# Optimization experiments

Measured on AMD Instinct MI355X. Metric: run time of the kernel, lower is better.

## Reference

```python
import jax, jax.numpy as jnp
import numpy as np

B, S, D, H = 2, 2048, 1024, 16
HD = D // H  # head size 64

def setup_inputs() -> dict:
    key = jax.random.key(0)
    ks = jax.random.split(key, 7)
    sc = 1.0 / np.sqrt(D)
    return {
        "batch_data": jax.random.normal(ks[0], (B, S, D), dtype=jnp.float32),
        "Wq": jax.random.normal(ks[1], (D, D), dtype=jnp.float32) * sc,
        "bq": jnp.zeros((D,), dtype=jnp.float32),
        "Wk": jax.random.normal(ks[2], (D, D), dtype=jnp.float32) * sc,
        "bk": jnp.zeros((D,), dtype=jnp.float32),
        "Wv": jax.random.normal(ks[3], (D, D), dtype=jnp.float32) * sc,
        "bv": jnp.zeros((D,), dtype=jnp.float32),
    }

def _split_heads(x):
    # [B,S,D] -> [B,H,S,HD]
    b, s, _ = x.shape
    return x.reshape(b, s, H, HD).transpose(0, 2, 1, 3)

def reference(batch_data, Wq, bq, Wk, bk, Wv, bv):
    q = _split_heads(batch_data @ Wq + bq)
    k = _split_heads(batch_data @ Wk + bk)
    v = _split_heads(batch_data @ Wv + bv)
    scores = jnp.einsum('bhqd,bhkd->bhqk', q, k) / jnp.sqrt(jnp.float32(HD))
    probs = jax.nn.softmax(scores, axis=-1)
    ctx = jnp.einsum('bhqk,bhkd->bhqd', probs, v)  # [B,H,S,HD]
    ctx = ctx.transpose(0, 2, 1, 3).reshape(batch_data.shape[0], batch_data.shape[1], D)
    return jnp.mean(ctx, axis=1)  # mean pool over sequence -> [B,D]
```

## Files before the change

### kernel.cpp

```cpp
#include <hip/hip_runtime.h>
#include <hip/hip_bf16.h>
#include <stdint.h>

#define B_  2
#define S_  2048
#define D_  1024
#define H_  16
#define HD_ 64

typedef __attribute__((ext_vector_type(8)))  __bf16 bf16x8;
typedef __attribute__((ext_vector_type(4)))  __bf16 bf16x4;
typedef __attribute__((ext_vector_type(2)))  __bf16 bf16x2;
typedef __attribute__((ext_vector_type(4)))  short  s16x4;
typedef __attribute__((ext_vector_type(8)))  short  s16x8;
typedef __attribute__((ext_vector_type(2)))  float  f32x2;
typedef __attribute__((ext_vector_type(4)))  float  f32x4;
typedef __attribute__((ext_vector_type(16))) float  f32x16;
typedef __attribute__((ext_vector_type(4)))  uint32_t u32x4;

#define QSCALE 0.18033688011112042f

__device__ __forceinline__ void gload16(const void* g, void* l) {
  __builtin_amdgcn_global_load_lds(
      (__attribute__((address_space(1))) void*)(uintptr_t)g,
      (__attribute__((address_space(3))) void*)(uintptr_t)l,
      16, 0, 0);
}

__device__ __forceinline__ bf16x8 cat8(s16x4 a, s16x4 b) {
  return __builtin_bit_cast(
      bf16x8, (s16x8)__builtin_shufflevector(a, b, 0, 1, 2, 3, 4, 5, 6, 7));
}

__global__ __launch_bounds__(256) void prep(
    const float* __restrict__ x, const float* __restrict__ wq,
    const float* __restrict__ wk, const float* __restrict__ wv,
    __bf16* __restrict__ xb, __bf16* __restrict__ wt, float* __restrict__ out) {
  __shared__ float tile[32][33];
  const int t = threadIdx.x;
  const int bx = blockIdx.x;
  if (bx < 4096) {
    int i = bx * 256 + t;
    float4 v = ((const float4*)x)[i];
    bf16x4 o;
    o[0] = (__bf16)v.x; o[1] = (__bf16)v.y; o[2] = (__bf16)v.z; o[3] = (__bf16)v.w;
    ((bf16x4*)xb)[i] = o;
  } else if (bx < 7168) {
    int tb = bx - 4096;
    int z = tb >> 10;
    int rem = tb & 1023;
    int n0 = (rem & 31) * 32, k0 = (rem >> 5) * 32;
    const float* w = (z == 0) ? wq : (z == 1 ? wk : wv);
    __bf16* o = wt + (size_t)z * D_ * D_;
    int tx = t & 31, ty = t >> 5;
    for (int i = 0; i < 4; ++i)
      tile[ty + 8 * i][tx] = w[(size_t)(k0 + ty + 8 * i) * D_ + n0 + tx];
    __syncthreads();
    for (int i = 0; i < 4; ++i)
      o[(size_t)(n0 + ty + 8 * i) * D_ + k0 + tx] = (__bf16)tile[tx][ty + 8 * i];
  } else {
    float4* o4 = (float4*)out;
    float4 z4 = {0.f, 0.f, 0.f, 0.f};
    o4[t] = z4;
    o4[t + 256] = z4;
  }
}

__global__ __launch_bounds__(256, 3) void gemm_qkv(
    const __bf16* __restrict__ xb, const __bf16* __restrict__ wt,
    const float* __restrict__ bq, const float* __restrict__ bk,
    const float* __restrict__ bv, __bf16* __restrict__ qh,
    __bf16* __restrict__ kh, __bf16* __restrict__ vt) {
  constexpr int K = 1024;
  constexpr int NIT = K / 32;
  __shared__ __attribute__((aligned(16))) __bf16 lA[2][128 * 32];
  __shared__ __attribute__((aligned(16))) __bf16 lB[2][128 * 32];

  const int z = blockIdx.z;
  const __bf16* w = wt + (size_t)z * K * D_;
  const float* bias = (z == 0) ? bq : (z == 1 ? bk : bv);
  const int t = threadIdx.x;
  const int lane = t & 63;
  const int wid = t >> 6;
  const int quad = lane >> 4;
  const int col = lane & 15;
  const int m0 = blockIdx.x * 128;
  const int n0 = blockIdx.y * 128;
  const int wr = (wid >> 1) * 64;
  const int wc = (wid & 1) * 64;

  const int sr0 = t >> 2;
  const int gc = (t & 3) ^ ((t >> 2) & 3);

  auto stage = [&](int kt, int buf) {
    gload16(xb + (size_t)(m0 + sr0) * K + kt * 32 + gc * 8,
            (char*)&lA[buf][0] + t * 16);
    gload16(xb + (size_t)(m0 + 64 + sr0) * K + kt * 32 + gc * 8,
            (char*)&lA[buf][0] + 4096 + t * 16);
    gload16(w + (size_t)(n0 + sr0) * K + kt * 32 + gc * 8,
            (char*)&lB[buf][0] + t * 16);
    gload16(w + (size_t)(n0 + 64 + sr0) * K + kt * 32 + gc * 8,
            (char*)&lB[buf][0] + 4096 + t * 16);
  };

  f32x4 acc[4][4] = {};

  stage(0, 0);

  if (z < 2) {
    for (int kt = 0; kt < NIT; ++kt) {
      const int cur = kt & 1;
      __syncthreads();
      if (kt + 1 < NIT) stage(kt + 1, cur ^ 1);
      bf16x8 fw[4], fx[4];
      for (int i = 0; i < 4; ++i) {
        int n = wr + i * 16 + col;
        int sl = quad ^ (n & 3);
        fw[i] = *(const bf16x8*)((const char*)&lB[cur][0] + n * 64 + sl * 16);
      }
      for (int j = 0; j < 4; ++j) {
        int m = wc + j * 16 + col;
        int sl = quad ^ (m & 3);
        fx[j] = *(const bf16x8*)((const char*)&lA[cur][0] + m * 64 + sl * 16);
      }
      for (int i = 0; i < 4; ++i)
        for (int j = 0; j < 4; ++j)
          acc[i][j] = __builtin_amdgcn_mfma_f32_16x16x32_bf16(
              fw[i], fx[j], acc[i][j], 0, 0, 0);
    }
    const float scale = (z == 0) ? QSCALE : 1.0f;
    __bf16* dst = (z == 0) ? qh : kh;
    for (int i = 0; i < 4; ++i) {
      int gnb = n0 + wr + i * 16 + quad * 4;
      float4 bi = *(const float4*)(bias + gnb);
      int h = gnb >> 6, hd = gnb & 63;
      for (int j = 0; j < 4; ++j) {
        int gm = m0 + wc + j * 16 + col;
        int b = gm >> 11, s = gm & 2047;
        bf16x4 pk;
        pk[0] = (__bf16)((acc[i][j][0] + bi.x) * scale);
        pk[1] = (__bf16)((acc[i][j][1] + bi.y) * scale);
        pk[2] = (__bf16)((acc[i][j][2] + bi.z) * scale);
        pk[3] = (__bf16)((acc[i][j][3] + bi.w) * scale);
        *(bf16x4*)(dst + ((size_t)(b * H_ + h) * S_ + s) * HD_ + hd) = pk;
      }
    }
  } else {
    for (int kt = 0; kt < NIT; ++kt) {
      const int cur = kt & 1;
      __syncthreads();
      if (kt + 1 < NIT) stage(kt + 1, cur ^ 1);
      bf16x8 fx[4], fw[4];
      for (int i = 0; i < 4; ++i) {
        int m = wr + i * 16 + col;
        int sl = quad ^ (m & 3);
        fx[i] = *(const bf16x8*)((const char*)&lA[cur][0] + m * 64 + sl * 16);
      }
      for (int j = 0; j < 4; ++j) {
        int n = wc + j * 16 + col;
        int sl = quad ^ (n & 3);
        fw[j] = *(const bf16x8*)((const char*)&lB[cur][0] + n * 64 + sl * 16);
      }
      for (int i = 0; i < 4; ++i)
        for (int j = 0; j < 4; ++j)
          acc[i][j] = __builtin_amdgcn_mfma_f32_16x16x32_bf16(
              fx[i], fw[j], acc[i][j], 0, 0, 0);
    }
    for (int i = 0; i < 4; ++i) {
      int gmb = m0 + wr + i * 16 + quad * 4;
      int b = gmb >> 11, s = gmb & 2047;
      for (int j = 0; j < 4; ++j) {
        int gn = n0 + wc + j * 16 + col;
        int h = gn >> 6, hd = gn & 63;
        float bi = bias[gn];
        bf16x4 pk;
        pk[0] = (__bf16)(acc[i][j][0] + bi);
        pk[1] = (__bf16)(acc[i][j][1] + bi);
        pk[2] = (__bf16)(acc[i][j][2] + bi);
        pk[3] = (__bf16)(acc[i][j][3] + bi);
        *(bf16x4*)(vt + ((size_t)(b * H_ + h) * HD_ + hd) * S_ + s) = pk;
      }
    }
  }
}

__global__ __launch_bounds__(256, 2) void attn1(
    const __bf16* __restrict__ qh, const __bf16* __restrict__ kh,
    const __bf16* __restrict__ vt, __bf16* __restrict__ po,
    float* __restrict__ pl) {
  __shared__ __attribute__((aligned(16))) __bf16 lK[2][64 * 64];
  __shared__ __attribute__((aligned(16))) __bf16 lV[2][64 * 64];

  const int t = threadIdx.x;
  const int lane = t & 63;
  const int half = lane >> 5;
  const int q31 = lane & 31;
  const int bh = blockIdx.x;
  const int kc = blockIdx.z;
  const int q0w = blockIdx.y * 256 + (t >> 6) * 64;

  const __bf16* qbase = qh + (size_t)bh * S_ * HD_;
  const __bf16* kbase = kh + (size_t)bh * S_ * HD_;
  const __bf16* vbase = vt + (size_t)bh * HD_ * S_;

  bf16x8 aq[2][4];
  for (int qt = 0; qt < 2; ++qt)
    for (int ks = 0; ks < 4; ++ks)
      aq[qt][ks] = *(const bf16x8*)(qbase +
          (size_t)(q0w + qt * 32 + q31) * HD_ + ks * 16 + half * 8);

  f32x16 o[2][2] = {};
  f32x2 ls[2] = {{0.f, 0.f}, {0.f, 0.f}};

  const int srow = t >> 3;
  const int sgc = (t & 7) ^ (srow & 7);

  auto stage = [&](int kt, int buf) {
    gload16(kbase + (size_t)(kt * 64 + srow) * HD_ + sgc * 8,
            (char*)&lK[buf][0] + t * 16);
    gload16(kbase + (size_t)(kt * 64 + 32 + srow) * HD_ + sgc * 8,
            (char*)&lK[buf][0] + 4096 + t * 16);
    gload16(vbase + (size_t)srow * S_ + kt * 64 + sgc * 8,
            (char*)&lV[buf][0] + t * 16);
    gload16(vbase + (size_t)(32 + srow) * S_ + kt * 64 + sgc * 8,
            (char*)&lV[buf][0] + 4096 + t * 16);
  };

  stage(kc * 16, 0);

  for (int kt0 = 0; kt0 < 16; ++kt0) {
    const int cur = kt0 & 1;
    __syncthreads();
    if (kt0 + 1 < 16) stage(kc * 16 + kt0 + 1, cur ^ 1);

    bf16x8 fk[2][4];
    s16x4  fv[2][2][4];
#pragma unroll
    for (int st = 0; st < 2; ++st) {
      const int row = st * 32 + q31;
#pragma unroll
      for (int ks = 0; ks < 4; ++ks) {
        int pos = (2 * ks + half) ^ (row & 7);
        fk[st][ks] = *(const bf16x8*)((const char*)&lK[cur][0] + row * 128 + pos * 16);
      }
    }
#pragma unroll
    for (int st = 0; st < 2; ++st)
#pragma unroll
      for (int hdt = 0; hdt < 2; ++hdt) {
        const int rowv = hdt * 32 + q31;
#pragma unroll
        for (int g = 0; g < 4; ++g) {
          int pos = (4 * st + g) ^ (rowv & 7);
          fv[st][hdt][g] = *(const s16x4*)((const char*)&lV[cur][0] + rowv * 128 +
                                           pos * 16 + half * 8);
        }
      }

#pragma unroll
    for (int st = 0; st < 2; ++st) {
      f32x16 sc0 = {}, sc1 = {};
#pragma unroll
      for (int ks = 0; ks < 4; ++ks) {
        sc0 = __builtin_amdgcn_mfma_f32_32x32x16_bf16(fk[st][ks], aq[0][ks], sc0, 0, 0, 0);
        sc1 = __builtin_amdgcn_mfma_f32_32x32x16_bf16(fk[st][ks], aq[1][ks], sc1, 0, 0, 0);
      }

      uint32_t pk0[8], pk1[8];
#pragma unroll
      for (int p = 0; p < 8; ++p) {
        float ea = __builtin_amdgcn_exp2f(sc0[2 * p]);
        float eb = __builtin_amdgcn_exp2f(sc0[2 * p + 1]);
        f32x2 e2 = {ea, eb};
        ls[0] += e2;
        uint32_t au = __builtin_bit_cast(uint32_t, ea) + 0x8000u;
        uint32_t bu = __builtin_bit_cast(uint32_t, eb) + 0x8000u;
        pk0[p] = __builtin_amdgcn_perm(bu, au, 0x07060302u);
      }
#pragma unroll
      for (int p = 0; p < 8; ++p) {
        float ea = __builtin_amdgcn_exp2f(sc1[2 * p]);
        float eb = __builtin_amdgcn_exp2f(sc1[2 * p + 1]);
        f32x2 e2 = {ea, eb};
        ls[1] += e2;
        uint32_t au = __builtin_bit_cast(uint32_t, ea) + 0x8000u;
        uint32_t bu = __builtin_bit_cast(uint32_t, eb) + 0x8000u;
        pk1[p] = __builtin_amdgcn_perm(bu, au, 0x07060302u);
      }

      u32x4 w;
      w[0] = pk0[0]; w[1] = pk0[1]; w[2] = pk0[2]; w[3] = pk0[3];
      bf16x8 fp0a = __builtin_bit_cast(bf16x8, w);
      w[0] = pk0[4]; w[1] = pk0[5]; w[2] = pk0[6]; w[3] = pk0[7];
      bf16x8 fp0b = __builtin_bit_cast(bf16x8, w);
      w[0] = pk1[0]; w[1] = pk1[1]; w[2] = pk1[2]; w[3] = pk1[3];
      bf16x8 fp1a = __builtin_bit_cast(bf16x8, w);
      w[0] = pk1[4]; w[1] = pk1[5]; w[2] = pk1[6]; w[3] = pk1[7];
      bf16x8 fp1b = __builtin_bit_cast(bf16x8, w);

#pragma unroll
      for (int hdt = 0; hdt < 2; ++hdt) {
        bf16x8 av0 = cat8(fv[st][hdt][0], fv[st][hdt][1]);
        bf16x8 av1 = cat8(fv[st][hdt][2], fv[st][hdt][3]);
        o[0][hdt] = __builtin_amdgcn_mfma_f32_32x32x16_bf16(av0, fp0a, o[0][hdt], 0, 0, 0);
        o[1][hdt] = __builtin_amdgcn_mfma_f32_32x32x16_bf16(av0, fp1a, o[1][hdt], 0, 0, 0);
        o[0][hdt] = __builtin_amdgcn_mfma_f32_32x32x16_bf16(av1, fp0b, o[0][hdt], 0, 0, 0);
        o[1][hdt] = __builtin_amdgcn_mfma_f32_32x32x16_bf16(av1, fp1b, o[1][hdt], 0, 0, 0);
      }
    }
  }

  const size_t slab = (size_t)(kc * 32 + bh) * S_;
  for (int qt = 0; qt < 2; ++qt) {
    float lq = ls[qt].x + ls[qt].y;
    float ltot = lq + __shfl_xor(lq, 32);
    const int qrow = q0w + qt * 32 + q31;
    if (half == 0) pl[slab + qrow] = ltot;
    for (int hdt = 0; hdt < 2; ++hdt)
      for (int rq = 0; rq < 4; ++rq) {
        bf16x4 pk;
        pk[0] = (__bf16)o[qt][hdt][rq * 4 + 0];
        pk[1] = (__bf16)o[qt][hdt][rq * 4 + 1];
        pk[2] = (__bf16)o[qt][hdt][rq * 4 + 2];
        pk[3] = (__bf16)o[qt][hdt][rq * 4 + 3];
        *(bf16x4*)(po + (slab + qrow) * HD_ + hdt * 32 + rq * 8 + half * 4) = pk;
      }
  }
}

__global__ __launch_bounds__(256) void attn2(const __bf16* __restrict__ po,
                                             const float* __restrict__ pl,
                                             float* __restrict__ out) {
  __shared__ float red[256];
  const int t = threadIdx.x;
  const int hd = t & 63;
  const int rgrp = t >> 6;
  const int bh = blockIdx.y;
  const int r0 = blockIdx.x * 64 + rgrp * 16;
  const size_t s0 = (size_t)bh * S_;
  const size_t s1 = (size_t)(32 + bh) * S_;
  float acc = 0.f;
#pragma unroll 4
  for (int i = 0; i < 16; ++i) {
    int row = r0 + i;
    float l = pl[s0 + row] + pl[s1 + row];
    float v = (float)po[(s0 + row) * HD_ + hd] +
              (float)po[(s1 + row) * HD_ + hd];
    acc += v / l;
  }
  red[t] = acc;
  __syncthreads();
  if (t < 64) {
    float s = red[t] + red[t + 64] + red[t + 128] + red[t + 192];
    atomicAdd(out + (size_t)(bh >> 4) * D_ + (bh & 15) * HD_ + hd,
              s * (1.0f / S_));
  }
}

extern "C" void kernel_launch(void* const* d_in, const int* in_sizes, int n_in,
                              void* d_out, int out_size, void* d_ws, size_t ws_size,
                              hipStream_t stream) {
  const float* x  = (const float*)d_in[0];
  const float* Wq = (const float*)d_in[1];
  const float* bq = (const float*)d_in[2];
  const float* Wk = (const float*)d_in[3];
  const float* bk = (const float*)d_in[4];
  const float* Wv = (const float*)d_in[5];
  const float* bv = (const float*)d_in[6];
  float* out = (float*)d_out;

  char* ws = (char*)d_ws;
  __bf16* qh = (__bf16*)(ws);
  __bf16* kh = (__bf16*)(ws + ((size_t)8  << 20));
  __bf16* vt = (__bf16*)(ws + ((size_t)16 << 20));
  __bf16* xb = (__bf16*)(ws + ((size_t)24 << 20));
  __bf16* wt = (__bf16*)(ws + ((size_t)32 << 20));
  __bf16* po = (__bf16*)(ws + ((size_t)24 << 20));
  float*  pl = (float*) (ws + ((size_t)40 << 20));

  prep<<<dim3(7169), dim3(256), 0, stream>>>(x, Wq, Wk, Wv, xb, wt, out);
  gemm_qkv<<<dim3(32, 8, 3), dim3(256), 0, stream>>>(xb, wt, bq, bk, bv, qh, kh, vt);
  attn1<<<dim3(B_ * H_, 8, 2), dim3(256), 0, stream>>>(qh, kh, vt, po, pl);
  attn2<<<dim3(32, B_ * H_), dim3(256), 0, stream>>>(po, pl, out);
}
```

Baseline: 160.0 us.

## Stage 128-key tiles per barrier in attention and raise MFMA issue priority

Result: no change. 162.8 us (+1.8%).

```diff
diff --git a/kernel.cpp b/kernel.cpp
--- a/kernel.cpp
+++ b/kernel.cpp
@@ -188,8 +188,8 @@
     const __bf16* __restrict__ qh, const __bf16* __restrict__ kh,
     const __bf16* __restrict__ vt, __bf16* __restrict__ po,
     float* __restrict__ pl) {
-  __shared__ __attribute__((aligned(16))) __bf16 lK[2][64 * 64];
-  __shared__ __attribute__((aligned(16))) __bf16 lV[2][64 * 64];
+  __shared__ __attribute__((aligned(16))) __bf16 lK[2][128 * 64];
+  __shared__ __attribute__((aligned(16))) __bf16 lV[2][64 * 128];
 
   const int t = threadIdx.x;
   const int lane = t & 63;
@@ -212,100 +212,109 @@
   f32x16 o[2][2] = {};
   f32x2 ls[2] = {{0.f, 0.f}, {0.f, 0.f}};
 
-  const int srow = t >> 3;
-  const int sgc = (t & 7) ^ (srow & 7);
+  const int rK = t >> 3;
+  const int cK = (t & 7) ^ (rK & 7);
+  const int rV = t >> 4;
+  const int cV = (t & 15) ^ (rV & 7);
 
   auto stage = [&](int kt, int buf) {
-    gload16(kbase + (size_t)(kt * 64 + srow) * HD_ + sgc * 8,
-            (char*)&lK[buf][0] + t * 16);
-    gload16(kbase + (size_t)(kt * 64 + 32 + srow) * HD_ + sgc * 8,
-            (char*)&lK[buf][0] + 4096 + t * 16);
-    gload16(vbase + (size_t)srow * S_ + kt * 64 + sgc * 8,
-            (char*)&lV[buf][0] + t * 16);
-    gload16(vbase + (size_t)(32 + srow) * S_ + kt * 64 + sgc * 8,
-            (char*)&lV[buf][0] + 4096 + t * 16);
+#pragma unroll
+    for (int i = 0; i < 4; ++i)
+      gload16(kbase + (size_t)(kt * 128 + i * 32 + rK) * HD_ + cK * 8,
+              (char*)&lK[buf][0] + i * 4096 + t * 16);
+#pragma unroll
+    for (int i = 0; i < 4; ++i)
+      gload16(vbase + (size_t)(i * 16 + rV) * S_ + kt * 128 + cV * 8,
+              (char*)&lV[buf][0] + i * 4096 + t * 16);
   };
 
-  stage(kc * 16, 0);
-
-  for (int kt0 = 0; kt0 < 16; ++kt0) {
-    const int cur = kt0 & 1;
+  stage(kc * 8, 0);
+
+  for (int it = 0; it < 8; ++it) {
+    const int cur = it & 1;
     __syncthreads();
-    if (kt0 + 1 < 16) stage(kc * 16 + kt0 + 1, cur ^ 1);
-
-    bf16x8 fk[2][4];
-    s16x4  fv[2][2][4];
-#pragma unroll
-    for (int st = 0; st < 2; ++st) {
-      const int row = st * 32 + q31;
-#pragma unroll
-      for (int ks = 0; ks < 4; ++ks) {
-        int pos = (2 * ks + half) ^ (row & 7);
-        fk[st][ks] = *(const bf16x8*)((const char*)&lK[cur][0] + row * 128 + pos * 16);
-      }
-    }
-#pragma unroll
-    for (int st = 0; st < 2; ++st)
-#pragma unroll
-      for (int hdt = 0; hdt < 2; ++hdt) {
-        const int rowv = hdt * 32 + q31;
-#pragma unroll
-        for (int g = 0; g < 4; ++g) {
-          int pos = (4 * st + g) ^ (rowv & 7);
-          fv[st][hdt][g] = *(const s16x4*)((const char*)&lV[cur][0] + rowv * 128 +
-                                           pos * 16 + half * 8);
-        }
-      }
-
-#pragma unroll
-    for (int st = 0; st < 2; ++st) {
-      f32x16 sc0 = {}, sc1 = {};
-#pragma unroll
-      for (int ks = 0; ks < 4; ++ks) {
-        sc0 = __builtin_amdgcn_mfma_f32_32x32x16_bf16(fk[st][ks], aq[0][ks], sc0, 0, 0, 0);
-        sc1 = __builtin_amdgcn_mfma_f32_32x32x16_bf16(fk[st][ks], aq[1][ks], sc1, 0, 0, 0);
-      }
-
-      uint32_t pk0[8], pk1[8];
-#pragma unroll
-      for (int p = 0; p < 8; ++p) {
-        float ea = __builtin_amdgcn_exp2f(sc0[2 * p]);
-        float eb = __builtin_amdgcn_exp2f(sc0[2 * p + 1]);
-        f32x2 e2 = {ea, eb};
-        ls[0] += e2;
-        uint32_t au = __builtin_bit_cast(uint32_t, ea) + 0x8000u;
-        uint32_t bu = __builtin_bit_cast(uint32_t, eb) + 0x8000u;
-        pk0[p] = __builtin_amdgcn_perm(bu, au, 0x07060302u);
-      }
-#pragma unroll
-      for (int p = 0; p < 8; ++p) {
-        float ea = __builtin_amdgcn_exp2f(sc1[2 * p]);
-        float eb = __builtin_amdgcn_exp2f(sc1[2 * p + 1]);
-        f32x2 e2 = {ea, eb};
-        ls[1] += e2;
-        uint32_t au = __builtin_bit_cast(uint32_t, ea) + 0x8000u;
-        uint32_t bu = __builtin_bit_cast(uint32_t, eb) + 0x8000u;
-        pk1[p] = __builtin_amdgcn_perm(bu, au, 0x07060302u);
-      }
-
-      u32x4 w;
-      w[0] = pk0[0]; w[1] = pk0[1]; w[2] = pk0[2]; w[3] = pk0[3];
-      bf16x8 fp0a = __builtin_bit_cast(bf16x8, w);
-      w[0] = pk0[4]; w[1] = pk0[5]; w[2] = pk0[6]; w[3] = pk0[7];
-      bf16x8 fp0b = __builtin_bit_cast(bf16x8, w);
-      w[0] = pk1[0]; w[1] = pk1[1]; w[2] = pk1[2]; w[3] = pk1[3];
-      bf16x8 fp1a = __builtin_bit_cast(bf16x8, w);
-      w[0] = pk1[4]; w[1] = pk1[5]; w[2] = pk1[6]; w[3] = pk1[7];
-      bf16x8 fp1b = __builtin_bit_cast(bf16x8, w);
-
-#pragma unroll
-      for (int hdt = 0; hdt < 2; ++hdt) {
-        bf16x8 av0 = cat8(fv[st][hdt][0], fv[st][hdt][1]);
-        bf16x8 av1 = cat8(fv[st][hdt][2], fv[st][hdt][3]);
-        o[0][hdt] = __builtin_amdgcn_mfma_f32_32x32x16_bf16(av0, fp0a, o[0][hdt], 0, 0, 0);
-        o[1][hdt] = __builtin_amdgcn_mfma_f32_32x32x16_bf16(av0, fp1a, o[1][hdt], 0, 0, 0);
-        o[0][hdt] = __builtin_amdgcn_mfma_f32_32x32x16_bf16(av1, fp0b, o[0][hdt], 0, 0, 0);
-        o[1][hdt] = __builtin_amdgcn_mfma_f32_32x32x16_bf16(av1, fp1b, o[1][hdt], 0, 0, 0);
+    if (it + 1 < 8) stage(kc * 8 + it + 1, cur ^ 1);
+
+#pragma unroll
+    for (int sub = 0; sub < 2; ++sub) {
+      bf16x8 fk[2][4];
+      s16x4  fv[2][2][4];
+#pragma unroll
+      for (int st = 0; st < 2; ++st) {
+        const int row = sub * 64 + st * 32 + q31;
+#pragma unroll
+        for (int ks = 0; ks < 4; ++ks) {
+          int pos = (2 * ks + half) ^ (q31 & 7);
+          fk[st][ks] = *(const bf16x8*)((const char*)&lK[cur][0] + row * 128 + pos * 16);
+        }
+      }
+#pragma unroll
+      for (int st = 0; st < 2; ++st)
+#pragma unroll
+        for (int hdt = 0; hdt < 2; ++hdt) {
+          const int rowv = hdt * 32 + q31;
+#pragma unroll
+          for (int g = 0; g < 4; ++g) {
+            int pos = (sub * 8 + 4 * st + g) ^ (q31 & 7);
+            fv[st][hdt][g] = *(const s16x4*)((const char*)&lV[cur][0] + rowv * 256 +
+                                             pos * 16 + half * 8);
+          }
+        }
+
+#pragma unroll
+      for (int st = 0; st < 2; ++st) {
+        f32x16 sc0 = {}, sc1 = {};
+        __builtin_amdgcn_s_setprio(1);
+#pragma unroll
+        for (int ks = 0; ks < 4; ++ks) {
+          sc0 = __builtin_amdgcn_mfma_f32_32x32x16_bf16(fk[st][ks], aq[0][ks], sc0, 0, 0, 0);
+          sc1 = __builtin_amdgcn_mfma_f32_32x32x16_bf16(fk[st][ks], aq[1][ks], sc1, 0, 0, 0);
+        }
+        __builtin_amdgcn_s_setprio(0);
+
+        uint32_t pk0[8], pk1[8];
+#pragma unroll
+        for (int p = 0; p < 8; ++p) {
+          float ea = __builtin_amdgcn_exp2f(sc0[2 * p]);
+          float eb = __builtin_amdgcn_exp2f(sc0[2 * p + 1]);
+          f32x2 e2 = {ea, eb};
+          ls[0] += e2;
+          uint32_t au = __builtin_bit_cast(uint32_t, ea) + 0x8000u;
+          uint32_t bu = __builtin_bit_cast(uint32_t, eb) + 0x8000u;
+          pk0[p] = __builtin_amdgcn_perm(bu, au, 0x07060302u);
+        }
+#pragma unroll
+        for (int p = 0; p < 8; ++p) {
+          float ea = __builtin_amdgcn_exp2f(sc1[2 * p]);
+          float eb = __builtin_amdgcn_exp2f(sc1[2 * p + 1]);
+          f32x2 e2 = {ea, eb};
+          ls[1] += e2;
+          uint32_t au = __builtin_bit_cast(uint32_t, ea) + 0x8000u;
+          uint32_t bu = __builtin_bit_cast(uint32_t, eb) + 0x8000u;
+          pk1[p] = __builtin_amdgcn_perm(bu, au, 0x07060302u);
+        }
+
+        u32x4 w;
+        w[0] = pk0[0]; w[1] = pk0[1]; w[2] = pk0[2]; w[3] = pk0[3];
+        bf16x8 fp0a = __builtin_bit_cast(bf16x8, w);
+        w[0] = pk0[4]; w[1] = pk0[5]; w[2] = pk0[6]; w[3] = pk0[7];
+        bf16x8 fp0b = __builtin_bit_cast(bf16x8, w);
+        w[0] = pk1[0]; w[1] = pk1[1]; w[2] = pk1[2]; w[3] = pk1[3];
+        bf16x8 fp1a = __builtin_bit_cast(bf16x8, w);
+        w[0] = pk1[4]; w[1] = pk1[5]; w[2] = pk1[6]; w[3] = pk1[7];
+        bf16x8 fp1b = __builtin_bit_cast(bf16x8, w);
+
+        __builtin_amdgcn_s_setprio(1);
+#pragma unroll
+        for (int hdt = 0; hdt < 2; ++hdt) {
+          bf16x8 av0 = cat8(fv[st][hdt][0], fv[st][hdt][1]);
+          bf16x8 av1 = cat8(fv[st][hdt][2], fv[st][hdt][3]);
+          o[0][hdt] = __builtin_amdgcn_mfma_f32_32x32x16_bf16(av0, fp0a, o[0][hdt], 0, 0, 0);
+          o[1][hdt] = __builtin_amdgcn_mfma_f32_32x32x16_bf16(av0, fp1a, o[1][hdt], 0, 0, 0);
+          o[0][hdt] = __builtin_amdgcn_mfma_f32_32x32x16_bf16(av1, fp0b, o[0][hdt], 0, 0, 0);
+          o[1][hdt] = __builtin_amdgcn_mfma_f32_32x32x16_bf16(av1, fp1b, o[1][hdt], 0, 0, 0);
+        }
+        __builtin_amdgcn_s_setprio(0);
       }
     }
   }
```

## Software-pipeline QK^T MFMA with softmax and PV of previous sub-tile

Applied to the files above, without the earlier changes.

New measurement: 161.5 us. Within noise of the previous version (+1.0%).

```diff
diff --git a/kernel.cpp b/kernel.cpp
--- a/kernel.cpp
+++ b/kernel.cpp
@@ -10,7 +10,6 @@
 
 typedef __attribute__((ext_vector_type(8)))  __bf16 bf16x8;
 typedef __attribute__((ext_vector_type(4)))  __bf16 bf16x4;
-typedef __attribute__((ext_vector_type(2)))  __bf16 bf16x2;
 typedef __attribute__((ext_vector_type(4)))  short  s16x4;
 typedef __attribute__((ext_vector_type(8)))  short  s16x8;
 typedef __attribute__((ext_vector_type(2)))  float  f32x2;
@@ -31,6 +30,7 @@
   return __builtin_bit_cast(
       bf16x8, (s16x8)__builtin_shufflevector(a, b, 0, 1, 2, 3, 4, 5, 6, 7));
 }
+
 
 __global__ __launch_bounds__(256) void prep(
     const float* __restrict__ x, const float* __restrict__ wq,
@@ -226,89 +226,112 @@
             (char*)&lV[buf][0] + 4096 + t * 16);
   };
 
+  auto read_fk = [&](int cur, int st, bf16x8 (&fk)[4]) {
+    const int row = st * 32 + q31;
+#pragma unroll
+    for (int ks = 0; ks < 4; ++ks) {
+      int pos = (2 * ks + half) ^ (q31 & 7);
+      fk[ks] = *(const bf16x8*)((const char*)&lK[cur][0] + row * 128 + pos * 16);
+    }
+  };
+
+  auto read_fv = [&](int cur, int st, s16x4 (&fv)[2][4]) {
+#pragma unroll
+    for (int hdt = 0; hdt < 2; ++hdt) {
+      const int rowv = hdt * 32 + q31;
+#pragma unroll
+      for (int g = 0; g < 4; ++g) {
+        int pos = (4 * st + g) ^ (q31 & 7);
+        fv[hdt][g] = *(const s16x4*)((const char*)&lV[cur][0] + rowv * 128 +
+                                     pos * 16 + half * 8);
+      }
+    }
+  };
+
+  auto qk = [&](const bf16x8 (&fk)[4], f32x16& s0, f32x16& s1) {
+    s0 = (f32x16){};
+    s1 = (f32x16){};
+#pragma unroll
+    for (int ks = 0; ks < 4; ++ks) {
+      s0 = __builtin_amdgcn_mfma_f32_32x32x16_bf16(fk[ks], aq[0][ks], s0, 0, 0, 0);
+      s1 = __builtin_amdgcn_mfma_f32_32x32x16_bf16(fk[ks], aq[1][ks], s1, 0, 0, 0);
+    }
+  };
+
+  auto sm_pv = [&](const f32x16& s0, const f32x16& s1, const s16x4 (&fv)[2][4]) {
+    uint32_t pk0[8], pk1[8];
+#pragma unroll
+    for (int p = 0; p < 8; ++p) {
+      float ea = __builtin_amdgcn_exp2f(s0[2 * p]);
+      float eb = __builtin_amdgcn_exp2f(s0[2 * p + 1]);
+      f32x2 e2 = {ea, eb};
+      ls[0] += e2;
+      uint32_t au = __builtin_bit_cast(uint32_t, ea) + 0x8000u;
+      uint32_t bu = __builtin_bit_cast(uint32_t, eb) + 0x8000u;
+      pk0[p] = __builtin_amdgcn_perm(bu, au, 0x07060302u);
+    }
+#pragma unroll
+    for (int p = 0; p < 8; ++p) {
+      float ea = __builtin_amdgcn_exp2f(s1[2 * p]);
+      float eb = __builtin_amdgcn_exp2f(s1[2 * p + 1]);
+      f32x2 e2 = {ea, eb};
+      ls[1] += e2;
+      uint32_t au = __builtin_bit_cast(uint32_t, ea) + 0x8000u;
+      uint32_t bu = __builtin_bit_cast(uint32_t, eb) + 0x8000u;
+      pk1[p] = __builtin_amdgcn_perm(bu, au, 0x07060302u);
+    }
+
+    u32x4 w;
+    w[0] = pk0[0]; w[1] = pk0[1]; w[2] = pk0[2]; w[3] = pk0[3];
+    bf16x8 fp0a = __builtin_bit_cast(bf16x8, w);
+    w[0] = pk0[4]; w[1] = pk0[5]; w[2] = pk0[6]; w[3] = pk0[7];
+    bf16x8 fp0b = __builtin_bit_cast(bf16x8, w);
+    w[0] = pk1[0]; w[1] = pk1[1]; w[2] = pk1[2]; w[3] = pk1[3];
+    bf16x8 fp1a = __builtin_bit_cast(bf16x8, w);
+    w[0] = pk1[4]; w[1] = pk1[5]; w[2] = pk1[6]; w[3] = pk1[7];
+    bf16x8 fp1b = __builtin_bit_cast(bf16x8, w);
+
+#pragma unroll
+    for (int hdt = 0; hdt < 2; ++hdt) {
+      bf16x8 av0 = cat8(fv[hdt][0], fv[hdt][1]);
+      bf16x8 av1 = cat8(fv[hdt][2], fv[hdt][3]);
+      o[0][hdt] = __builtin_amdgcn_mfma_f32_32x32x16_bf16(av0, fp0a, o[0][hdt], 0, 0, 0);
+      o[1][hdt] = __builtin_amdgcn_mfma_f32_32x32x16_bf16(av0, fp1a, o[1][hdt], 0, 0, 0);
+      o[0][hdt] = __builtin_amdgcn_mfma_f32_32x32x16_bf16(av1, fp0b, o[0][hdt], 0, 0, 0);
+      o[1][hdt] = __builtin_amdgcn_mfma_f32_32x32x16_bf16(av1, fp1b, o[1][hdt], 0, 0, 0);
+    }
+  };
+
   stage(kc * 16, 0);
-
-  for (int kt0 = 0; kt0 < 16; ++kt0) {
+  __syncthreads();
+  stage(kc * 16 + 1, 1);
+
+  bf16x8 fk[4];
+  s16x4 fvp[2][4];
+  f32x16 s0c, s1c;
+
+  read_fk(0, 0, fk);
+  read_fv(0, 0, fvp);
+  qk(fk, s0c, s1c);
+
+  read_fk(0, 1, fk);
+  sm_pv(s0c, s1c, fvp);
+  read_fv(0, 1, fvp);
+  qk(fk, s0c, s1c);
+
+  for (int kt0 = 1; kt0 < 16; ++kt0) {
     const int cur = kt0 & 1;
     __syncthreads();
     if (kt0 + 1 < 16) stage(kc * 16 + kt0 + 1, cur ^ 1);
-
-    bf16x8 fk[2][4];
-    s16x4  fv[2][2][4];
 #pragma unroll
     for (int st = 0; st < 2; ++st) {
-      const int row = st * 32 + q31;
-#pragma unroll
-      for (int ks = 0; ks < 4; ++ks) {
-        int pos = (2 * ks + half) ^ (row & 7);
-        fk[st][ks] = *(const bf16x8*)((const char*)&lK[cur][0] + row * 128 + pos * 16);
-      }
-    }
-#pragma unroll
-    for (int st = 0; st < 2; ++st)
-#pragma unroll
-      for (int hdt = 0; hdt < 2; ++hdt) {
-        const int rowv = hdt * 32 + q31;
-#pragma unroll
-        for (int g = 0; g < 4; ++g) {
-          int pos = (4 * st + g) ^ (rowv & 7);
-          fv[st][hdt][g] = *(const s16x4*)((const char*)&lV[cur][0] + rowv * 128 +
-                                           pos * 16 + half * 8);
-        }
-      }
-
-#pragma unroll
-    for (int st = 0; st < 2; ++st) {
-      f32x16 sc0 = {}, sc1 = {};
-#pragma unroll
-      for (int ks = 0; ks < 4; ++ks) {
-        sc0 = __builtin_amdgcn_mfma_f32_32x32x16_bf16(fk[st][ks], aq[0][ks], sc0, 0, 0, 0);
-        sc1 = __builtin_amdgcn_mfma_f32_32x32x16_bf16(fk[st][ks], aq[1][ks], sc1, 0, 0, 0);
-      }
-
-      uint32_t pk0[8], pk1[8];
-#pragma unroll
-      for (int p = 0; p < 8; ++p) {
-        float ea = __builtin_amdgcn_exp2f(sc0[2 * p]);
-        float eb = __builtin_amdgcn_exp2f(sc0[2 * p + 1]);
-        f32x2 e2 = {ea, eb};
-        ls[0] += e2;
-        uint32_t au = __builtin_bit_cast(uint32_t, ea) + 0x8000u;
-        uint32_t bu = __builtin_bit_cast(uint32_t, eb) + 0x8000u;
-        pk0[p] = __builtin_amdgcn_perm(bu, au, 0x07060302u);
-      }
-#pragma unroll
-      for (int p = 0; p < 8; ++p) {
-        float ea = __builtin_amdgcn_exp2f(sc1[2 * p]);
-        float eb = __builtin_amdgcn_exp2f(sc1[2 * p + 1]);
-        f32x2 e2 = {ea, eb};
-        ls[1] += e2;
-        uint32_t au = __builtin_bit_cast(uint32_t, ea) + 0x8000u;
-        uint32_t bu = __builtin_bit_cast(uint32_t, eb) + 0x8000u;
-        pk1[p] = __builtin_amdgcn_perm(bu, au, 0x07060302u);
-      }
-
-      u32x4 w;
-      w[0] = pk0[0]; w[1] = pk0[1]; w[2] = pk0[2]; w[3] = pk0[3];
-      bf16x8 fp0a = __builtin_bit_cast(bf16x8, w);
-      w[0] = pk0[4]; w[1] = pk0[5]; w[2] = pk0[6]; w[3] = pk0[7];
-      bf16x8 fp0b = __builtin_bit_cast(bf16x8, w);
-      w[0] = pk1[0]; w[1] = pk1[1]; w[2] = pk1[2]; w[3] = pk1[3];
-      bf16x8 fp1a = __builtin_bit_cast(bf16x8, w);
-      w[0] = pk1[4]; w[1] = pk1[5]; w[2] = pk1[6]; w[3] = pk1[7];
-      bf16x8 fp1b = __builtin_bit_cast(bf16x8, w);
-
-#pragma unroll
-      for (int hdt = 0; hdt < 2; ++hdt) {
-        bf16x8 av0 = cat8(fv[st][hdt][0], fv[st][hdt][1]);
-        bf16x8 av1 = cat8(fv[st][hdt][2], fv[st][hdt][3]);
-        o[0][hdt] = __builtin_amdgcn_mfma_f32_32x32x16_bf16(av0, fp0a, o[0][hdt], 0, 0, 0);
-        o[1][hdt] = __builtin_amdgcn_mfma_f32_32x32x16_bf16(av0, fp1a, o[1][hdt], 0, 0, 0);
-        o[0][hdt] = __builtin_amdgcn_mfma_f32_32x32x16_bf16(av1, fp0b, o[0][hdt], 0, 0, 0);
-        o[1][hdt] = __builtin_amdgcn_mfma_f32_32x32x16_bf16(av1, fp1b, o[1][hdt], 0, 0, 0);
-      }
-    }
-  }
+      read_fk(cur, st, fk);
+      sm_pv(s0c, s1c, fvp);
+      read_fv(cur, st, fvp);
+      qk(fk, s0c, s1c);
+    }
+  }
+  sm_pv(s0c, s1c, fvp);
 
   const size_t slab = (size_t)(kc * 32 + bh) * S_;
   for (int qt = 0; qt < 2; ++qt) {
```
